# Kernel tuning notes

Hardware: AMD Instinct MI355X
Metric: run time of the kernel (lower is better)

## Reference

```python
import jax, jax.numpy as jnp
import numpy as np

N, E, H, L, G = 50000, 500000, 128, 4, 1000
EPS = 1e-7      # GENConv message eps
LN_EPS = 1e-5   # torch LayerNorm default


def setup_inputs() -> dict:
    key = jax.random.key(0)
    ks = jax.random.split(key, 24)
    d = {}
    d["x"] = jax.random.normal(ks[0], (N, 9), jnp.float32)
    d["edge_index"] = jax.random.randint(ks[1], (2, E), 0, N, jnp.int32)
    d["edge_attr"] = jax.random.normal(ks[2], (E, 3), jnp.float32)
    d["batch"] = jnp.sort(jax.random.randint(ks[3], (N,), 0, G, jnp.int32))
    s9, s3, sh, s2h = 1/np.sqrt(9), 1/np.sqrt(3), 1/np.sqrt(H), 1/np.sqrt(2*H)
    u = lambda k, shp, s: jax.random.uniform(k, shp, jnp.float32, -s, s)
    d["enc_node_W"] = u(ks[4], (9, H), s9)
    d["enc_node_b"] = u(ks[5], (H,), s9)
    d["enc_edge_W"] = u(ks[6], (3, H), s3)
    d["enc_edge_b"] = u(ks[7], (H,), s3)
    d["ln_g"] = jnp.ones((L, H), jnp.float32)   # DeepGCNLayer pre-norm affine
    d["ln_b"] = jnp.zeros((L, H), jnp.float32)
    d["W1"] = u(ks[8], (L, H, 2*H), sh)          # GENConv MLP layer 1
    d["b1"] = u(ks[9], (L, 2*H), sh)
    d["mlp_ln_g"] = jnp.ones((L, 2*H), jnp.float32)
    d["mlp_ln_b"] = jnp.zeros((L, 2*H), jnp.float32)
    d["W2"] = u(ks[10], (L, 2*H, H), s2h)        # GENConv MLP layer 2
    d["b2"] = u(ks[11], (L, H), s2h)
    d["t"] = jnp.ones((L,), jnp.float32)         # learnable softmax temperature, init 1.0
    return d


def layernorm(x, g, b):
    mu = x.mean(-1, keepdims=True)
    var = ((x - mu) ** 2).mean(-1, keepdims=True)
    return (x - mu) / jnp.sqrt(var + LN_EPS) * g + b


def genconv(h, src, dst, ea, t, W1, b1, lg, lb, W2, b2):
    # message: relu(x_j + edge_attr) + eps   -> [E, H]
    msg = jax.nn.relu(h[src] + ea) + EPS
    # softmax aggregation over incoming edges, per channel
    logits = t * msg
    m = jax.ops.segment_max(logits, dst, num_segments=N)
    num = jnp.exp(logits - m[dst])
    den = jax.ops.segment_sum(num, dst, num_segments=N)
    alpha = num / den[dst]
    agg = jax.ops.segment_sum(msg * alpha, dst, num_segments=N)
    out = agg + h  # root residual inside GENConv
    z = jax.nn.relu(layernorm(out @ W1 + b1, lg, lb))
    return z @ W2 + b2


def reference(x, edge_index, edge_attr, batch, enc_node_W, enc_node_b,
              enc_edge_W, enc_edge_b, ln_g, ln_b, W1, b1, mlp_ln_g, mlp_ln_b,
              W2, b2, t):
    src, dst = edge_index[0], edge_index[1]
    h = x @ enc_node_W + enc_node_b            # node encoder  [N, H]
    ea = edge_attr @ enc_edge_W + enc_edge_b   # edge encoder  [E, H]
    # layer 0: conv only (DeeperGCN forward uses layers[0].conv directly)
    h = genconv(h, src, dst, ea, t[0], W1[0], b1[0], mlp_ln_g[0], mlp_ln_b[0], W2[0], b2[0])
    # layers 1..L-1: res+ block: x + conv(relu(LN(x))); dropout is identity (eval)
    for i in range(1, L):
        z = jax.nn.relu(layernorm(h, ln_g[i], ln_b[i]))
        h = h + genconv(z, src, dst, ea, t[i], W1[i], b1[i], mlp_ln_g[i], mlp_ln_b[i], W2[i], b2[i])
    h = jax.nn.relu(layernorm(h, ln_g[0], ln_b[0]))  # reuses layer-0 norm
    # global mean pool over graphs
    counts = jax.ops.segment_sum(jnp.ones((N,), h.dtype), batch, num_segments=G)
    sums = jax.ops.segment_sum(h, batch, num_segments=G)
    return sums / jnp.maximum(counts, 1.0)[:, None]
```

## Files before the change

### kernel.cpp

```cpp
#include <hip/hip_runtime.h>

#define NN 50000
#define NE 500000
#define HD 128
#define HD2 256
#define NL 4
#define NG 1000

constexpr float MSG_EPS = 1e-7f;
constexpr float LNEPS   = 1e-5f;
constexpr float LOG2E   = 1.4426950408889634f;

typedef float  f32x4  __attribute__((ext_vector_type(4)));
typedef float  f32x2  __attribute__((ext_vector_type(2)));
typedef __bf16 bf16x8 __attribute__((ext_vector_type(8)));

__device__ __forceinline__ unsigned short f2b(float f) {
    unsigned int u = __float_as_uint(f);
    unsigned int r = u + 0x7FFFu + ((u >> 16) & 1u);
    return (unsigned short)(r >> 16);
}
__device__ __forceinline__ float b2f(unsigned short h) {
    return __uint_as_float(((unsigned int)h) << 16);
}
__device__ __forceinline__ unsigned int pack2(float a, float b) {
    return (unsigned int)f2b(a) | ((unsigned int)f2b(b) << 16);
}

#define PREP_BLKS 512
#define ENC_BLKS 25000
#define HIST_BLKS ((NE + 255) / 256)

__global__ void k_setup(const float* __restrict__ x, const float* __restrict__ encW,
                        const float* __restrict__ encB, unsigned short* __restrict__ zb,
                        const float* __restrict__ W1, const float* __restrict__ W2,
                        unsigned short* __restrict__ W1T, unsigned short* __restrict__ W2T,
                        const int* __restrict__ dst, int* __restrict__ counts) {
    int bid = blockIdx.x, tid = threadIdx.x;
    if (bid < PREP_BLKS) {
        int idx = bid * 256 + tid;
        {
            int k = idx & 127, n = (idx >> 7) & 255, l = idx >> 15;
            W1T[idx] = f2b(W1[(l * 128 + k) * 256 + n]);
        }
        {
            int k = idx & 255, n = (idx >> 8) & 127, l = idx >> 15;
            W2T[idx] = f2b(W2[(l * 256 + k) * 128 + n]);
        }
    } else if (bid < PREP_BLKS + ENC_BLKS) {
        int n = (bid - PREP_BLKS) * 2 + (tid >> 7);
        int c = tid & 127;
        float xr[9];
#pragma unroll
        for (int k = 0; k < 9; k++) xr[k] = x[n * 9 + k];
        float acc = encB[c];
#pragma unroll
        for (int k = 0; k < 9; k++) acc = fmaf(xr[k], encW[k * HD + c], acc);
        zb[(size_t)n * HD + c] = f2b(acc);
    } else {
        int e = (bid - PREP_BLKS - ENC_BLKS) * 256 + tid;
        if (e < NE) atomicAdd(&counts[dst[e]], 1);
    }
}

#define SCAN_B 512
#define NSB ((NN + SCAN_B - 1) / SCAN_B)

__global__ void k_scan1(const int* __restrict__ counts, int* __restrict__ incl,
                        int* __restrict__ bsum) {
    __shared__ int s[SCAN_B];
    int i = blockIdx.x * SCAN_B + threadIdx.x;
    int v = (i < NN) ? counts[i] : 0;
    s[threadIdx.x] = v;
    __syncthreads();
    for (int off = 1; off < SCAN_B; off <<= 1) {
        int t = (threadIdx.x >= off) ? s[threadIdx.x - off] : 0;
        __syncthreads();
        s[threadIdx.x] += t;
        __syncthreads();
    }
    if (i < NN) incl[i] = s[threadIdx.x];
    if (threadIdx.x == SCAN_B - 1) bsum[blockIdx.x] = s[threadIdx.x];
}

__global__ void k_scan2(const int* __restrict__ bsum, int* __restrict__ boff, int nb) {
    __shared__ int s[128];
    int v = (threadIdx.x < nb) ? bsum[threadIdx.x] : 0;
    s[threadIdx.x] = v;
    __syncthreads();
    for (int off = 1; off < 128; off <<= 1) {
        int t = (threadIdx.x >= off) ? s[threadIdx.x - off] : 0;
        __syncthreads();
        s[threadIdx.x] += t;
        __syncthreads();
    }
    if (threadIdx.x < nb) boff[threadIdx.x] = s[threadIdx.x] - v;
}

__global__ void k_scan3g(const int* __restrict__ incl, const int* __restrict__ boff,
                         int* __restrict__ row_start, const int* __restrict__ batch,
                         int* __restrict__ gstart) {
    if (blockIdx.x < NSB) {
        int i = blockIdx.x * SCAN_B + threadIdx.x;
        if (i < NN) row_start[i + 1] = incl[i] + boff[blockIdx.x];
        if (i == 0) row_start[0] = 0;
    } else {
        int g = (blockIdx.x - NSB) * SCAN_B + threadIdx.x;
        if (g > NG) return;
        int lo = 0, hi = NN;
        while (lo < hi) {
            int mid = (lo + hi) >> 1;
            if (batch[mid] < g) lo = mid + 1;
            else hi = mid;
        }
        gstart[g] = lo;
    }
}

__global__ void k_scatter(const int* __restrict__ src, const int* __restrict__ dst,
                          const float* __restrict__ eattr, const int* __restrict__ row_start,
                          int* __restrict__ cursor, float4* __restrict__ aperm) {
    int e = blockIdx.x * blockDim.x + threadIdx.x;
    if (e >= NE) return;
    int d = dst[e];
    int p = row_start[d] + atomicAdd(&cursor[d], 1);
    float4 v;
    v.x = eattr[e * 3 + 0];
    v.y = eattr[e * 3 + 1];
    v.z = eattr[e * 3 + 2];
    v.w = __int_as_float(src[e]);
    aperm[p] = v;
}

__device__ __forceinline__ void edge_acc2(float4 a, unsigned int zz, f32x2 w0, f32x2 w1,
                                          f32x2 w2, f32x2 bb, float t2, f32x2& num,
                                          f32x2& wm) {
    f32x2 z;
    z.x = __uint_as_float(zz << 16);
    z.y = __uint_as_float(zz & 0xFFFF0000u);
    f32x2 m = z + bb + a.x * w0 + a.y * w1 + a.z * w2;
    m.x = fmaxf(m.x, 0.f);
    m.y = fmaxf(m.y, 0.f);
    f32x2 e;
    e.x = exp2f(t2 * m.x);
    e.y = exp2f(t2 * m.y);
    num += e;
    wm += m * e;
}

__global__ __launch_bounds__(256) void k_aggregate(const unsigned short* __restrict__ zbin,
                                                   const float4* __restrict__ aperm,
                                                   const int* __restrict__ row_start,
                                                   const float* __restrict__ We,
                                                   const float* __restrict__ be,
                                                   const float* __restrict__ t, int layer,
                                                   unsigned int* __restrict__ outb) {
    int w = threadIdx.x >> 6, lane = threadIdx.x & 63;
    int n = blockIdx.x * 4 + w;
    if (n >= NN) return;
    int c = lane * 2;
    f32x2 w0 = *(const f32x2*)&We[c];
    f32x2 w1 = *(const f32x2*)&We[HD + c];
    f32x2 w2 = *(const f32x2*)&We[2 * HD + c];
    f32x2 bb = *(const f32x2*)&be[c];
    float t2 = t[layer] * LOG2E;
    int s0 = __builtin_amdgcn_readfirstlane(row_start[n]);
    int s1 = __builtin_amdgcn_readfirstlane(row_start[n + 1]);
    f32x2 num = (f32x2){0.f, 0.f}, wm = (f32x2){0.f, 0.f};
    const unsigned int* z32 = (const unsigned int*)zbin;
    int p = s0;
    for (; p + 8 <= s1; p += 8) {
        float4 A[8];
#pragma unroll
        for (int j = 0; j < 8; j++) A[j] = aperm[p + j];
        unsigned int Z[8];
#pragma unroll
        for (int j = 0; j < 8; j++) {
            int sj = __builtin_amdgcn_readfirstlane(__float_as_int(A[j].w));
            Z[j] = z32[(size_t)sj * 64 + lane];
        }
#pragma unroll
        for (int j = 0; j < 8; j++) edge_acc2(A[j], Z[j], w0, w1, w2, bb, t2, num, wm);
    }
    for (; p + 4 <= s1; p += 4) {
        float4 A[4];
#pragma unroll
        for (int j = 0; j < 4; j++) A[j] = aperm[p + j];
        unsigned int Z[4];
#pragma unroll
        for (int j = 0; j < 4; j++) {
            int sj = __builtin_amdgcn_readfirstlane(__float_as_int(A[j].w));
            Z[j] = z32[(size_t)sj * 64 + lane];
        }
#pragma unroll
        for (int j = 0; j < 4; j++) edge_acc2(A[j], Z[j], w0, w1, w2, bb, t2, num, wm);
    }
    for (; p < s1; p++) {
        float4 a = aperm[p];
        int sj = __builtin_amdgcn_readfirstlane(__float_as_int(a.w));
        unsigned int zz = z32[(size_t)sj * 64 + lane];
        edge_acc2(a, zz, w0, w1, w2, bb, t2, num, wm);
    }
    unsigned int zn = z32[(size_t)n * 64 + lane];
    bool has = s1 > s0;
    float ox = (has ? (wm.x / num.x + MSG_EPS) : 0.f) + __uint_as_float(zn << 16);
    float oy = (has ? (wm.y / num.y + MSG_EPS) : 0.f) + __uint_as_float(zn & 0xFFFF0000u);
    outb[(size_t)n * 64 + lane] = pack2(ox, oy);
}

#define BM 16
#define HS_LD 264
#define HT_LD 136

__global__ __launch_bounds__(256) void k_mlp(const unsigned short* __restrict__ outb,
                                             const unsigned short* __restrict__ W1T,
                                             const float* __restrict__ b1l,
                                             const float* __restrict__ lgl,
                                             const float* __restrict__ lbl,
                                             const unsigned short* __restrict__ W2T,
                                             const float* __restrict__ b2l,
                                             unsigned short* __restrict__ h,
                                             const float* __restrict__ gn,
                                             const float* __restrict__ bn,
                                             unsigned short* __restrict__ zb,
                                             int add_residual) {
    __shared__ __align__(16) unsigned short Hs[BM * HS_LD];
    __shared__ __align__(16) unsigned short Ht[BM * HT_LD];
    __shared__ __align__(16) float2 st1[16][4];

    int nb = blockIdx.x * BM;
    int tid = threadIdx.x;
    int w = tid >> 6, lane = tid & 63, q = lane >> 4, i = lane & 15;

    f32x4 acc[4];
#pragma unroll
    for (int ct = 0; ct < 4; ct++) acc[ct] = (f32x4){0.f, 0.f, 0.f, 0.f};

    bf16x8 acur, bcur[4];
    acur = *(const bf16x8*)&outb[(size_t)(nb + i) * HD + q * 8];
#pragma unroll
    for (int ct = 0; ct < 4; ct++)
        bcur[ct] = *(const bf16x8*)&W1T[(w * 64 + ct * 16 + i) * HD + q * 8];

#pragma unroll
    for (int ks = 0; ks < 4; ks++) {
        bf16x8 anxt, bnxt[4];
        if (ks < 3) {
            anxt = *(const bf16x8*)&outb[(size_t)(nb + i) * HD + (ks + 1) * 32 + q * 8];
#pragma unroll
            for (int ct = 0; ct < 4; ct++)
                bnxt[ct] =
                    *(const bf16x8*)&W1T[(w * 64 + ct * 16 + i) * HD + (ks + 1) * 32 + q * 8];
        }
#pragma unroll
        for (int ct = 0; ct < 4; ct++)
            acc[ct] = __builtin_amdgcn_mfma_f32_16x16x32_bf16(acur, bcur[ct], acc[ct], 0, 0, 0);
        if (ks < 3) {
            acur = anxt;
#pragma unroll
            for (int ct = 0; ct < 4; ct++) bcur[ct] = bnxt[ct];
        }
    }

#pragma unroll
    for (int ct = 0; ct < 4; ct++) {
        float bb = b1l[w * 64 + ct * 16 + i];
#pragma unroll
        for (int r = 0; r < 4; r++) acc[ct][r] += bb;
    }

    {
        float sv[4], qv[4];
#pragma unroll
        for (int r = 0; r < 4; r++) {
            sv[r] = acc[0][r] + acc[1][r] + acc[2][r] + acc[3][r];
            float sq = 0.f;
#pragma unroll
            for (int ct = 0; ct < 4; ct++) sq = fmaf(acc[ct][r], acc[ct][r], sq);
            qv[r] = sq;
        }
#pragma unroll
        for (int m = 1; m <= 8; m <<= 1)
#pragma unroll
            for (int r = 0; r < 4; r++) {
                sv[r] += __shfl_xor(sv[r], m);
                qv[r] += __shfl_xor(qv[r], m);
            }
        if (i == 0) {
#pragma unroll
            for (int r = 0; r < 4; r++) st1[q * 4 + r][w] = make_float2(sv[r], qv[r]);
        }
    }
    __syncthreads();

    {
        float mu[4], inv[4];
#pragma unroll
        for (int r = 0; r < 4; r++) {
            const float4* sp = (const float4*)&st1[q * 4 + r][0];
            float4 a = sp[0], b = sp[1];
            float S = a.x + a.z + b.x + b.z;
            float Q = a.y + a.w + b.y + b.w;
            float m_ = S * (1.f / 256.f);
            float v_ = Q * (1.f / 256.f) - m_ * m_;
            mu[r] = m_;
            inv[r] = rsqrtf(v_ + LNEPS);
        }
#pragma unroll
        for (int ct = 0; ct < 4; ct++) {
            float g = lgl[w * 64 + ct * 16 + i];
            float c = lbl[w * 64 + ct * 16 + i];
#pragma unroll
            for (int r = 0; r < 4; r++) {
                float v = fmaxf(fmaf((acc[ct][r] - mu[r]) * inv[r], g, c), 0.f);
                Hs[(q * 4 + r) * HS_LD + w * 64 + ct * 16 + i] = f2b(v);
            }
        }
    }
    __syncthreads();

    f32x4 acc2[2];
#pragma unroll
    for (int ct = 0; ct < 2; ct++) acc2[ct] = (f32x4){0.f, 0.f, 0.f, 0.f};

    bf16x8 hc, bc[2];
    hc = *(const bf16x8*)&Hs[i * HS_LD + q * 8];
#pragma unroll
    for (int ct = 0; ct < 2; ct++)
        bc[ct] = *(const bf16x8*)&W2T[(w * 32 + ct * 16 + i) * HD2 + q * 8];

#pragma unroll
    for (int ks = 0; ks < 8; ks++) {
        bf16x8 hn, bn2[2];
        if (ks < 7) {
            hn = *(const bf16x8*)&Hs[i * HS_LD + (ks + 1) * 32 + q * 8];
#pragma unroll
            for (int ct = 0; ct < 2; ct++)
                bn2[ct] =
                    *(const bf16x8*)&W2T[(w * 32 + ct * 16 + i) * HD2 + (ks + 1) * 32 + q * 8];
        }
#pragma unroll
        for (int ct = 0; ct < 2; ct++)
            acc2[ct] = __builtin_amdgcn_mfma_f32_16x16x32_bf16(hc, bc[ct], acc2[ct], 0, 0, 0);
        if (ks < 7) {
            hc = hn;
#pragma unroll
            for (int ct = 0; ct < 2; ct++) bc[ct] = bn2[ct];
        }
    }

#pragma unroll
    for (int ct = 0; ct < 2; ct++) {
        float bb = b2l[w * 32 + ct * 16 + i];
#pragma unroll
        for (int r = 0; r < 4; r++)
            Ht[(q * 4 + r) * HT_LD + w * 32 + ct * 16 + i] = f2b(acc2[ct][r] + bb);
    }
    __syncthreads();

    {
        const unsigned int* Ht32 = (const unsigned int*)Ht;
        unsigned int* h32 = (unsigned int*)h;
        unsigned int* zb32 = (unsigned int*)zb;
        float2 gg = *(const float2*)&gn[lane * 2];
        float2 cc = *(const float2*)&bn[lane * 2];
#pragma unroll
        for (int k = 0; k < 4; k++) {
            int rr = w * 4 + k;
            int row = nb + rr;
            unsigned int tv = Ht32[rr * (HT_LD / 2) + lane];
            float cx = b2f((unsigned short)tv), cy = b2f((unsigned short)(tv >> 16));
            if (add_residual) {
                unsigned int hv = h32[(size_t)row * 64 + lane];
                cx += b2f((unsigned short)hv);
                cy += b2f((unsigned short)(hv >> 16));
            }
            h32[(size_t)row * 64 + lane] = pack2(cx, cy);
            float s = cx + cy, sq = cx * cx + cy * cy;
#pragma unroll
            for (int m = 32; m >= 1; m >>= 1) {
                s += __shfl_xor(s, m);
                sq += __shfl_xor(sq, m);
            }
            float mu = s * (1.f / 128.f);
            float var = sq * (1.f / 128.f) - mu * mu;
            float inv = rsqrtf(var + LNEPS);
            float z0 = fmaxf(fmaf((cx - mu) * inv, gg.x, cc.x), 0.f);
            float z1 = fmaxf(fmaf((cy - mu) * inv, gg.y, cc.y), 0.f);
            zb32[(size_t)row * 64 + lane] = pack2(z0, z1);
        }
    }
}

__global__ void k_pool(const unsigned short* __restrict__ zb, const int* __restrict__ gstart,
                       float* __restrict__ out) {
    int g = blockIdx.x;
    int c = threadIdx.x;
    int a = gstart[g], b = gstart[g + 1];
    float s0 = 0.f, s1 = 0.f;
    int n = a;
    for (; n + 2 <= b; n += 2) {
        s0 += b2f(zb[(size_t)n * HD + c]);
        s1 += b2f(zb[(size_t)(n + 1) * HD + c]);
    }
    if (n < b) s0 += b2f(zb[(size_t)n * HD + c]);
    out[g * HD + c] = (s0 + s1) / fmaxf((float)(b - a), 1.f);
}

extern "C" void kernel_launch(void* const* d_in, const int* in_sizes, int n_in, void* d_out,
                              int out_size, void* d_ws, size_t ws_size, hipStream_t stream) {
    const float* x     = (const float*)d_in[0];
    const int* ei      = (const int*)d_in[1];
    const float* eattr = (const float*)d_in[2];
    const int* batch   = (const int*)d_in[3];
    const float* encW  = (const float*)d_in[4];
    const float* encB  = (const float*)d_in[5];
    const float* eW    = (const float*)d_in[6];
    const float* eB    = (const float*)d_in[7];
    const float* ln_g  = (const float*)d_in[8];
    const float* ln_b  = (const float*)d_in[9];
    const float* W1    = (const float*)d_in[10];
    const float* b1    = (const float*)d_in[11];
    const float* mlg   = (const float*)d_in[12];
    const float* mlb   = (const float*)d_in[13];
    const float* W2    = (const float*)d_in[14];
    const float* b2    = (const float*)d_in[15];
    const float* t     = (const float*)d_in[16];
    const int* src = ei;
    const int* dst = ei + NE;

    char* w = (char*)d_ws;
    auto alloc = [&](size_t bytes) {
        char* p = w;
        w += (bytes + 255) & ~size_t(255);
        return p;
    };
    unsigned short* h    = (unsigned short*)alloc(sizeof(unsigned short) * NN * HD);
    unsigned short* zb   = (unsigned short*)alloc(sizeof(unsigned short) * NN * HD);
    unsigned int* outb   = (unsigned int*)alloc(sizeof(unsigned int) * NN * HD / 2);
    float4* aperm        = (float4*)alloc(sizeof(float4) * NE);
    int* row_start       = (int*)alloc(sizeof(int) * (NN + 1));
    int* counts          = (int*)alloc(sizeof(int) * NN);
    int* cursor          = (int*)alloc(sizeof(int) * NN);
    int* incl            = (int*)alloc(sizeof(int) * NN);
    int* bsum            = (int*)alloc(sizeof(int) * 128);
    int* boff            = (int*)alloc(sizeof(int) * 128);
    int* gstart          = (int*)alloc(sizeof(int) * (NG + 1));
    unsigned short* W1T  = (unsigned short*)alloc(sizeof(unsigned short) * NL * HD * HD2);
    unsigned short* W2T  = (unsigned short*)alloc(sizeof(unsigned short) * NL * HD2 * HD);

    hipMemsetAsync(counts, 0, sizeof(int) * NN, stream);
    hipMemsetAsync(cursor, 0, sizeof(int) * NN, stream);

    k_setup<<<PREP_BLKS + ENC_BLKS + HIST_BLKS, 256, 0, stream>>>(x, encW, encB, zb, W1, W2,
                                                                  W1T, W2T, dst, counts);
    k_scan1<<<NSB, SCAN_B, 0, stream>>>(counts, incl, bsum);
    k_scan2<<<1, 128, 0, stream>>>(bsum, boff, NSB);
    k_scan3g<<<NSB + 2, SCAN_B, 0, stream>>>(incl, boff, row_start, batch, gstart);
    k_scatter<<<(NE + 255) / 256, 256, 0, stream>>>(src, dst, eattr, row_start, cursor, aperm);

    for (int l = 0; l < NL; l++) {
        k_aggregate<<<(NN + 3) / 4, 256, 0, stream>>>(zb, aperm, row_start, eW, eB, t, l, outb);
        int ln_next = (l + 1) % NL;
        k_mlp<<<NN / BM, 256, 0, stream>>>(
            (const unsigned short*)outb, W1T + (size_t)l * HD * HD2, b1 + l * HD2,
            mlg + l * HD2, mlb + l * HD2, W2T + (size_t)l * HD2 * HD, b2 + l * HD, h,
            ln_g + ln_next * HD, ln_b + ln_next * HD, zb, l > 0);
    }
    k_pool<<<NG, HD, 0, stream>>>(zb, gstart, (float*)d_out);
}
```

Before: 555.4 us.

## Retile MLP kernel to 64-row blocks with 8 waves sharing weight fragments

New measurement: 543.2 us. 2.2% less time.

```diff
diff --git a/kernel.cpp b/kernel.cpp
--- a/kernel.cpp
+++ b/kernel.cpp
@@ -208,11 +208,11 @@
     outb[(size_t)n * 64 + lane] = pack2(ox, oy);
 }
 
-#define BM 16
+#define BM 64
 #define HS_LD 264
 #define HT_LD 136
 
-__global__ __launch_bounds__(256) void k_mlp(const unsigned short* __restrict__ outb,
+__global__ __launch_bounds__(512) void k_mlp(const unsigned short* __restrict__ outb,
                                              const unsigned short* __restrict__ W1T,
                                              const float* __restrict__ b1l,
                                              const float* __restrict__ lgl,
@@ -225,136 +225,143 @@
                                              unsigned short* __restrict__ zb,
                                              int add_residual) {
     __shared__ __align__(16) unsigned short Hs[BM * HS_LD];
-    __shared__ __align__(16) unsigned short Ht[BM * HT_LD];
-    __shared__ __align__(16) float2 st1[16][4];
+    __shared__ __align__(16) float2 st1[4][16][8];
 
     int nb = blockIdx.x * BM;
     int tid = threadIdx.x;
     int w = tid >> 6, lane = tid & 63, q = lane >> 4, i = lane & 15;
 
-    f32x4 acc[4];
-#pragma unroll
-    for (int ct = 0; ct < 4; ct++) acc[ct] = (f32x4){0.f, 0.f, 0.f, 0.f};
-
-    bf16x8 acur, bcur[4];
-    acur = *(const bf16x8*)&outb[(size_t)(nb + i) * HD + q * 8];
-#pragma unroll
-    for (int ct = 0; ct < 4; ct++)
-        bcur[ct] = *(const bf16x8*)&W1T[(w * 64 + ct * 16 + i) * HD + q * 8];
+    f32x4 acc[4][2];
+#pragma unroll
+    for (int rt = 0; rt < 4; rt++)
+#pragma unroll
+        for (int ct = 0; ct < 2; ct++) acc[rt][ct] = (f32x4){0.f, 0.f, 0.f, 0.f};
+
+    bf16x8 bcur[2];
+#pragma unroll
+    for (int ct = 0; ct < 2; ct++)
+        bcur[ct] = *(const bf16x8*)&W1T[(w * 32 + ct * 16 + i) * HD + q * 8];
 
 #pragma unroll
     for (int ks = 0; ks < 4; ks++) {
-        bf16x8 anxt, bnxt[4];
+        bf16x8 bnxt[2];
         if (ks < 3) {
-            anxt = *(const bf16x8*)&outb[(size_t)(nb + i) * HD + (ks + 1) * 32 + q * 8];
-#pragma unroll
-            for (int ct = 0; ct < 4; ct++)
+#pragma unroll
+            for (int ct = 0; ct < 2; ct++)
                 bnxt[ct] =
-                    *(const bf16x8*)&W1T[(w * 64 + ct * 16 + i) * HD + (ks + 1) * 32 + q * 8];
-        }
-#pragma unroll
-        for (int ct = 0; ct < 4; ct++)
-            acc[ct] = __builtin_amdgcn_mfma_f32_16x16x32_bf16(acur, bcur[ct], acc[ct], 0, 0, 0);
+                    *(const bf16x8*)&W1T[(w * 32 + ct * 16 + i) * HD + (ks + 1) * 32 + q * 8];
+        }
+#pragma unroll
+        for (int rt = 0; rt < 4; rt++) {
+            int row = nb + rt * 16 + i;
+            bf16x8 a = (row < NN) ? *(const bf16x8*)&outb[(size_t)row * HD + ks * 32 + q * 8]
+                                  : (bf16x8)(__bf16)0.f;
+#pragma unroll
+            for (int ct = 0; ct < 2; ct++)
+                acc[rt][ct] =
+                    __builtin_amdgcn_mfma_f32_16x16x32_bf16(a, bcur[ct], acc[rt][ct], 0, 0, 0);
+        }
         if (ks < 3) {
-            acur = anxt;
-#pragma unroll
-            for (int ct = 0; ct < 4; ct++) bcur[ct] = bnxt[ct];
-        }
-    }
-
-#pragma unroll
-    for (int ct = 0; ct < 4; ct++) {
-        float bb = b1l[w * 64 + ct * 16 + i];
-#pragma unroll
-        for (int r = 0; r < 4; r++) acc[ct][r] += bb;
+#pragma unroll
+            for (int ct = 0; ct < 2; ct++) bcur[ct] = bnxt[ct];
+        }
+    }
+
+#pragma unroll
+    for (int ct = 0; ct < 2; ct++) {
+        float bb = b1l[w * 32 + ct * 16 + i];
+#pragma unroll
+        for (int rt = 0; rt < 4; rt++)
+#pragma unroll
+            for (int r = 0; r < 4; r++) acc[rt][ct][r] += bb;
     }
 
     {
-        float sv[4], qv[4];
-#pragma unroll
-        for (int r = 0; r < 4; r++) {
-            sv[r] = acc[0][r] + acc[1][r] + acc[2][r] + acc[3][r];
-            float sq = 0.f;
-#pragma unroll
-            for (int ct = 0; ct < 4; ct++) sq = fmaf(acc[ct][r], acc[ct][r], sq);
-            qv[r] = sq;
-        }
+        float sv[4][4], qv[4][4];
+#pragma unroll
+        for (int rt = 0; rt < 4; rt++)
+#pragma unroll
+            for (int r = 0; r < 4; r++) {
+                sv[rt][r] = acc[rt][0][r] + acc[rt][1][r];
+                qv[rt][r] = fmaf(acc[rt][0][r], acc[rt][0][r],
+                                 acc[rt][1][r] * acc[rt][1][r]);
+            }
 #pragma unroll
         for (int m = 1; m <= 8; m <<= 1)
 #pragma unroll
+            for (int rt = 0; rt < 4; rt++)
+#pragma unroll
+                for (int r = 0; r < 4; r++) {
+                    sv[rt][r] += __shfl_xor(sv[rt][r], m);
+                    qv[rt][r] += __shfl_xor(qv[rt][r], m);
+                }
+        if (i == 0) {
+#pragma unroll
+            for (int rt = 0; rt < 4; rt++)
+#pragma unroll
+                for (int r = 0; r < 4; r++)
+                    st1[rt][q * 4 + r][w] = make_float2(sv[rt][r], qv[rt][r]);
+        }
+    }
+    __syncthreads();
+
+    {
+        float mu[4][4], inv[4][4];
+#pragma unroll
+        for (int rt = 0; rt < 4; rt++)
+#pragma unroll
             for (int r = 0; r < 4; r++) {
-                sv[r] += __shfl_xor(sv[r], m);
-                qv[r] += __shfl_xor(qv[r], m);
+                const float4* sp = (const float4*)&st1[rt][q * 4 + r][0];
+                float4 a = sp[0], b = sp[1], cc4 = sp[2], d4 = sp[3];
+                float S = a.x + a.z + b.x + b.z + cc4.x + cc4.z + d4.x + d4.z;
+                float Q = a.y + a.w + b.y + b.w + cc4.y + cc4.w + d4.y + d4.w;
+                float m_ = S * (1.f / 256.f);
+                float v_ = Q * (1.f / 256.f) - m_ * m_;
+                mu[rt][r] = m_;
+                inv[rt][r] = rsqrtf(v_ + LNEPS);
             }
-        if (i == 0) {
-#pragma unroll
-            for (int r = 0; r < 4; r++) st1[q * 4 + r][w] = make_float2(sv[r], qv[r]);
-        }
-    }
-    __syncthreads();
-
+#pragma unroll
+        for (int ct = 0; ct < 2; ct++) {
+            float g = lgl[w * 32 + ct * 16 + i];
+            float c = lbl[w * 32 + ct * 16 + i];
+#pragma unroll
+            for (int rt = 0; rt < 4; rt++)
+#pragma unroll
+                for (int r = 0; r < 4; r++) {
+                    float v =
+                        fmaxf(fmaf((acc[rt][ct][r] - mu[rt][r]) * inv[rt][r], g, c), 0.f);
+                    Hs[(rt * 16 + q * 4 + r) * HS_LD + w * 32 + ct * 16 + i] = f2b(v);
+                }
+        }
+    }
+    __syncthreads();
+
+    f32x4 acc2[4];
+#pragma unroll
+    for (int rt = 0; rt < 4; rt++) acc2[rt] = (f32x4){0.f, 0.f, 0.f, 0.f};
+
+    bf16x8 bc = *(const bf16x8*)&W2T[(w * 16 + i) * HD2 + q * 8];
+#pragma unroll
+    for (int ks = 0; ks < 8; ks++) {
+        bf16x8 bn2;
+        if (ks < 7) bn2 = *(const bf16x8*)&W2T[(w * 16 + i) * HD2 + (ks + 1) * 32 + q * 8];
+#pragma unroll
+        for (int rt = 0; rt < 4; rt++) {
+            bf16x8 a = *(const bf16x8*)&Hs[(rt * 16 + i) * HS_LD + ks * 32 + q * 8];
+            acc2[rt] = __builtin_amdgcn_mfma_f32_16x16x32_bf16(a, bc, acc2[rt], 0, 0, 0);
+        }
+        if (ks < 7) bc = bn2;
+    }
+    __syncthreads();
+
+    unsigned short* Ht = Hs;
     {
-        float mu[4], inv[4];
-#pragma unroll
-        for (int r = 0; r < 4; r++) {
-            const float4* sp = (const float4*)&st1[q * 4 + r][0];
-            float4 a = sp[0], b = sp[1];
-            float S = a.x + a.z + b.x + b.z;
-            float Q = a.y + a.w + b.y + b.w;
-            float m_ = S * (1.f / 256.f);
-            float v_ = Q * (1.f / 256.f) - m_ * m_;
-            mu[r] = m_;
-            inv[r] = rsqrtf(v_ + LNEPS);
-        }
-#pragma unroll
-        for (int ct = 0; ct < 4; ct++) {
-            float g = lgl[w * 64 + ct * 16 + i];
-            float c = lbl[w * 64 + ct * 16 + i];
-#pragma unroll
-            for (int r = 0; r < 4; r++) {
-                float v = fmaxf(fmaf((acc[ct][r] - mu[r]) * inv[r], g, c), 0.f);
-                Hs[(q * 4 + r) * HS_LD + w * 64 + ct * 16 + i] = f2b(v);
-            }
-        }
-    }
-    __syncthreads();
-
-    f32x4 acc2[2];
-#pragma unroll
-    for (int ct = 0; ct < 2; ct++) acc2[ct] = (f32x4){0.f, 0.f, 0.f, 0.f};
-
-    bf16x8 hc, bc[2];
-    hc = *(const bf16x8*)&Hs[i * HS_LD + q * 8];
-#pragma unroll
-    for (int ct = 0; ct < 2; ct++)
-        bc[ct] = *(const bf16x8*)&W2T[(w * 32 + ct * 16 + i) * HD2 + q * 8];
-
-#pragma unroll
-    for (int ks = 0; ks < 8; ks++) {
-        bf16x8 hn, bn2[2];
-        if (ks < 7) {
-            hn = *(const bf16x8*)&Hs[i * HS_LD + (ks + 1) * 32 + q * 8];
-#pragma unroll
-            for (int ct = 0; ct < 2; ct++)
-                bn2[ct] =
-                    *(const bf16x8*)&W2T[(w * 32 + ct * 16 + i) * HD2 + (ks + 1) * 32 + q * 8];
-        }
-#pragma unroll
-        for (int ct = 0; ct < 2; ct++)
-            acc2[ct] = __builtin_amdgcn_mfma_f32_16x16x32_bf16(hc, bc[ct], acc2[ct], 0, 0, 0);
-        if (ks < 7) {
-            hc = hn;
-#pragma unroll
-            for (int ct = 0; ct < 2; ct++) bc[ct] = bn2[ct];
-        }
-    }
-
-#pragma unroll
-    for (int ct = 0; ct < 2; ct++) {
-        float bb = b2l[w * 32 + ct * 16 + i];
-#pragma unroll
-        for (int r = 0; r < 4; r++)
-            Ht[(q * 4 + r) * HT_LD + w * 32 + ct * 16 + i] = f2b(acc2[ct][r] + bb);
+        float bb = b2l[w * 16 + i];
+#pragma unroll
+        for (int rt = 0; rt < 4; rt++)
+#pragma unroll
+            for (int r = 0; r < 4; r++)
+                Ht[(rt * 16 + q * 4 + r) * HT_LD + w * 16 + i] = f2b(acc2[rt][r] + bb);
     }
     __syncthreads();
 
@@ -365,9 +372,10 @@
         float2 gg = *(const float2*)&gn[lane * 2];
         float2 cc = *(const float2*)&bn[lane * 2];
 #pragma unroll
-        for (int k = 0; k < 4; k++) {
-            int rr = w * 4 + k;
+        for (int k = 0; k < 8; k++) {
+            int rr = w * 8 + k;
             int row = nb + rr;
+            if (row >= NN) break;
             unsigned int tv = Ht32[rr * (HT_LD / 2) + lane];
             float cx = b2f((unsigned short)tv), cy = b2f((unsigned short)(tv >> 16));
             if (add_residual) {
@@ -462,7 +470,7 @@
     for (int l = 0; l < NL; l++) {
         k_aggregate<<<(NN + 3) / 4, 256, 0, stream>>>(zb, aperm, row_start, eW, eB, t, l, outb);
         int ln_next = (l + 1) % NL;
-        k_mlp<<<NN / BM, 256, 0, stream>>>(
+        k_mlp<<<(NN + BM - 1) / BM, 512, 0, stream>>>(
             (const unsigned short*)outb, W1T + (size_t)l * HD * HD2, b1 + l * HD2,
             mlg + l * HD2, mlb + l * HD2, W2T + (size_t)l * HD2 * HD, b2 + l * HD, h,
             ln_g + ln_next * HD, ln_b + ln_next * HD, zb, l > 0);
```
